# Optimization experiments

Measured on AMD Instinct MI355X. Metric: run time of the kernel, lower is better.

## Reference

```python
import jax, jax.numpy as jnp
import numpy as np

K = 3
UP_H, UP_W = 120, 160  # up_size
RES_H, RES_W = UP_H + K - 1, UP_W + K - 1  # bilinear target before valid depthwise conv


def _bilinear_align_corners(x, out_h, out_w):
    """PyTorch UpsamplingBilinear2d (align_corners=True). x: [B,C,H,W]."""
    B, C, H, W = x.shape
    # row interpolation
    hy = jnp.arange(out_h, dtype=x.dtype) * ((H - 1) / (out_h - 1))
    y0 = jnp.floor(hy).astype(jnp.int32)
    y1 = jnp.minimum(y0 + 1, H - 1)
    fy = (hy - y0.astype(x.dtype))[None, None, :, None]
    x = x[:, :, y0, :] * (1 - fy) + x[:, :, y1, :] * fy  # [B,C,out_h,W]
    # col interpolation
    wx = jnp.arange(out_w, dtype=x.dtype) * ((W - 1) / (out_w - 1))
    x0i = jnp.floor(wx).astype(jnp.int32)
    x1i = jnp.minimum(x0i + 1, W - 1)
    fx = (wx - x0i.astype(x.dtype))[None, None, None, :]
    return x[:, :, :, x0i] * (1 - fx) + x[:, :, :, x1i] * fx  # [B,C,out_h,out_w]


def setup_inputs() -> dict:
    key = jax.random.key(0)
    k1, k2, k3 = jax.random.split(key, 3)
    C_in, C_out = 256, 128
    x = jax.random.normal(k1, (8, C_in, 60, 80), dtype=jnp.float32)
    # depthwise kernel [C_in, 1, K, K], pointwise [C_out, C_in]; fan-in-ish scale
    w_dw = jax.random.normal(k2, (C_in, 1, K, K), dtype=jnp.float32) * (1.0 / K)
    w_pw = jax.random.normal(k3, (C_out, C_in), dtype=jnp.float32) * (1.0 / np.sqrt(C_in))
    return {"x": x, "w_dw": w_dw, "w_pw": w_pw}


def reference(x, w_dw, w_pw):
    C_in = x.shape[1]
    # 1) bilinear upsample (align_corners=True) to (UP_H+K-1, UP_W+K-1)
    up = _bilinear_align_corners(x, RES_H, RES_W)
    # 2) depthwise KxK conv, stride 1, VALID padding -> [B,C_in,UP_H,UP_W]
    dw = jax.lax.conv_general_dilated(
        up, w_dw, window_strides=(1, 1), padding="VALID",
        dimension_numbers=("NCHW", "OIHW", "NCHW"),
        feature_group_count=C_in)
    # 3) pointwise 1x1 conv -> [B,C_out,UP_H,UP_W]
    return jnp.einsum("bchw,oc->bohw", dw, w_pw)
```

## Files before the change

kernel.cpp:

```cpp
#include <hip/hip_runtime.h>

#define CIN  256
#define HIN  60
#define WIN  80
#define UPH  120
#define UPW  160
#define COUT 128
#define NPIX (UPH*UPW)

typedef __bf16 bf16x2 __attribute__((ext_vector_type(2)));
typedef __bf16 bf16x8 __attribute__((ext_vector_type(8)));
typedef float  floatx4 __attribute__((ext_vector_type(4)));

#define A_NT 320
#define A_XR 5
#define A_CP 17
#define A_AS 49

__global__ __launch_bounds__(A_NT, 5) void dw_kernel(
    const float* __restrict__ x,
    const float* __restrict__ wdw,
    __bf16* __restrict__ dwb,
    int b0)
{
    __shared__ bf16x2 s_px[A_XR * 84 * A_CP];
    __shared__ float  s_A[16 * A_AS];

    const int tid = threadIdx.x;
    const int h0  = blockIdx.x * 4;
    const int cb  = blockIdx.y * 16;
    const int bl  = blockIdx.z;
    const int b   = b0 + bl;

    const float HS = 59.0f / 121.0f;
    const float WS = 79.0f / 161.0f;
    const int rbase = (int)(h0 * HS);

    const float* xb = x + ((size_t)b * CIN + cb) * (HIN * WIN);
    #pragma unroll
    for (int k = 0; k < 6; k++) {
        int i = tid + k * A_NT;
        if (i < 1680) {
            int ch  = i / 105;
            int rem = i - ch * 105;
            int r   = rem / 21;
            int c4  = rem - r * 21;
            int gy  = min(rbase + r, HIN - 1);
            const float* xrow = xb + (size_t)ch * (HIN * WIN) + gy * WIN;
            int base = (r * 84 + c4 * 4) * A_CP + ch;
            if (c4 < 20) {
                float4 v = *(const float4*)(xrow + c4 * 4);
                float x5 = xrow[min(c4 * 4 + 4, WIN - 1)];
                s_px[base]          = (bf16x2){(__bf16)v.x, (__bf16)v.y};
                s_px[base + A_CP]   = (bf16x2){(__bf16)v.y, (__bf16)v.z};
                s_px[base + 2*A_CP] = (bf16x2){(__bf16)v.z, (__bf16)v.w};
                s_px[base + 3*A_CP] = (bf16x2){(__bf16)v.w, (__bf16)x5};
            } else {
                float v = xrow[WIN - 1];
                bf16x2 p = {(__bf16)v, (__bf16)v};
                s_px[base]          = p;
                s_px[base + A_CP]   = p;
                s_px[base + 2*A_CP] = p;
                s_px[base + 3*A_CP] = p;
            }
        }
    }
    for (int i = tid; i < 16 * 4 * 9; i += A_NT) {
        int ch  = i / 36;
        int rem = i - ch * 36;
        int h   = rem / 9;
        int dyj = rem - h * 9;
        int dy  = dyj / 3;
        int j   = dyj - dy * 3;
        int ybh = (int)((h0 + h) * HS);
        float acc = 0.f;
        #pragma unroll
        for (int i3 = 0; i3 < 3; i3++) {
            float hy = (h0 + h + i3) * HS;
            int y0 = (int)hy;
            float fy = hy - (float)y0;
            int y1 = min(y0 + 1, HIN - 1);
            float wgt = ((y0 - ybh) == dy ? (1.f - fy) : 0.f)
                      + ((y1 - ybh) == dy ? fy : 0.f);
            acc = fmaf(wgt, wdw[(cb + ch) * 9 + i3 * 3 + j], acc);
        }
        s_A[ch * A_AS + h * 12 + dy * 4 + j] = acc;
    }
    __syncthreads();

    const int ch  = tid & 15;
    const int rid = tid >> 4;
    const int wq  = rid * 8;
    int rbh[4];
    #pragma unroll
    for (int hh = 0; hh < 4; hh++)
        rbh[hh] = (int)((h0 + hh) * HS) - rbase;

    float fx[10]; int wi[10];
    #pragma unroll
    for (int j = 0; j < 10; j++) {
        float wx = (float)(wq + j) * WS;
        int x0 = (int)wx;
        fx[j] = wx - (float)x0;
        wi[j] = x0 * A_CP + ch;
    }

    float d[4][8];
    #pragma unroll
    for (int hh = 0; hh < 4; hh++)
        #pragma unroll
        for (int i = 0; i < 8; i++) d[hh][i] = 0.f;

    #pragma unroll
    for (int r = 0; r < A_XR; r++) {
        float cx[10];
        #pragma unroll
        for (int j = 0; j < 10; j++) {
            bf16x2 p = s_px[r * 84 * A_CP + wi[j]];
            float lo = (float)p[0], hi = (float)p[1];
            cx[j] = fmaf(fx[j], hi - lo, lo);
        }
        #pragma unroll
        for (int hh = 0; hh < 4; hh++) {
            int dyL = r - rbh[hh];
            if ((unsigned)dyL <= 2u) {
                const float* Ab = &s_A[ch * A_AS + hh * 12 + dyL * 4];
                float A0 = Ab[0], A1 = Ab[1], A2 = Ab[2];
                #pragma unroll
                for (int i = 0; i < 8; i++)
                    d[hh][i] = fmaf(A0, cx[i],
                               fmaf(A1, cx[i+1],
                               fmaf(A2, cx[i+2], d[hh][i])));
            }
        }
    }
    #pragma unroll
    for (int hh = 0; hh < 4; hh++) {
        bf16x8 o;
        #pragma unroll
        for (int i = 0; i < 8; i++) o[i] = (__bf16)d[hh][i];
        size_t off = ((size_t)bl * CIN + cb + ch) * NPIX
                   + (size_t)(h0 + hh) * UPW + wq;
        *(bf16x8*)(dwb + off) = o;
    }
}

#define B_NT 512
#define B_WS 264
#define B_DS 40

__global__ __launch_bounds__(B_NT, 4) void pw_kernel(
    const __bf16* __restrict__ dwb,
    const float* __restrict__ wpw,
    float* __restrict__ out,
    int b0)
{
    __shared__ __align__(16) __bf16 s_wpw[COUT * B_WS];
    __shared__ __align__(16) __bf16 s_dw[128 * B_DS];

    const int tid  = threadIdx.x;
    const int tile = blockIdx.x;
    const int bl   = blockIdx.y;
    const int b    = b0 + bl;

    {
        const int o = tid >> 2, seg = tid & 3;
        #pragma unroll
        for (int q = 0; q < 8; q++) {
            int c0 = seg * 64 + q * 8;
            float4 v0 = *(const float4*)(wpw + (size_t)o * CIN + c0);
            float4 v1 = *(const float4*)(wpw + (size_t)o * CIN + c0 + 4);
            bf16x8 f = {(__bf16)v0.x, (__bf16)v0.y, (__bf16)v0.z, (__bf16)v0.w,
                        (__bf16)v1.x, (__bf16)v1.y, (__bf16)v1.z, (__bf16)v1.w};
            *(bf16x8*)&s_wpw[o * B_WS + c0] = f;
        }
    }

    const int wave = tid >> 6, lane = tid & 63;
    const int quad = lane >> 4, l16 = lane & 15;
    const int o32  = (wave & 3) * 32;
    const int pg   = wave >> 2;

    floatx4 acc[2][4];
    #pragma unroll
    for (int a = 0; a < 2; a++)
        #pragma unroll
        for (int p = 0; p < 4; p++) acc[a][p] = (floatx4){0.f,0.f,0.f,0.f};

    const __bf16* dwbase = dwb + (size_t)bl * CIN * NPIX + tile * 128;
    const int cS = tid & 31, p8 = tid >> 5;

    bf16x8 v = *(const bf16x8*)(dwbase + (size_t)cS * NPIX + p8 * 8);

    for (int ck = 0; ck < 8; ck++) {
        __syncthreads();
        #pragma unroll
        for (int i = 0; i < 8; i++)
            s_dw[(p8 * 8 + i) * B_DS + cS] = v[i];
        __syncthreads();

        if (ck < 7)
            v = *(const bf16x8*)(dwbase + (size_t)((ck+1) * 32 + cS) * NPIX + p8 * 8);

        bf16x8 af0 = *(const bf16x8*)&s_wpw[(o32 + l16) * B_WS + ck * 32 + quad * 8];
        bf16x8 af1 = *(const bf16x8*)&s_wpw[(o32 + 16 + l16) * B_WS + ck * 32 + quad * 8];
        #pragma unroll
        for (int pt = 0; pt < 4; pt++) {
            bf16x8 bf = *(const bf16x8*)&s_dw[(pg * 64 + pt * 16 + l16) * B_DS + quad * 8];
            acc[0][pt] = __builtin_amdgcn_mfma_f32_16x16x32_bf16(af0, bf, acc[0][pt], 0, 0, 0);
            acc[1][pt] = __builtin_amdgcn_mfma_f32_16x16x32_bf16(af1, bf, acc[1][pt], 0, 0, 0);
        }
    }

    float* ob = out + (size_t)b * COUT * NPIX + tile * 128;
    #pragma unroll
    for (int ot = 0; ot < 2; ot++)
        #pragma unroll
        for (int pt = 0; pt < 4; pt++)
            #pragma unroll
            for (int r = 0; r < 4; r++)
                ob[(size_t)(o32 + ot * 16 + quad * 4 + r) * NPIX
                   + pg * 64 + pt * 16 + l16] = acc[ot][pt][r];
}

extern "C" void kernel_launch(void* const* d_in, const int* in_sizes, int n_in,
                              void* d_out, int out_size, void* d_ws, size_t ws_size,
                              hipStream_t stream) {
    const float* x   = (const float*)d_in[0];
    const float* wdw = (const float*)d_in[1];
    const float* wpw = (const float*)d_in[2];
    float* out = (float*)d_out;
    __bf16* dwb = (__bf16*)d_ws;

    int bs = 8;
    while (bs > 1 && (size_t)bs * CIN * NPIX * 2 > ws_size) bs >>= 1;

    for (int b0 = 0; b0 < 8; b0 += bs) {
        dim3 gA(30, CIN / 16, bs);
        dw_kernel<<<gA, A_NT, 0, stream>>>(x, wdw, dwb, b0);
        dim3 gB(NPIX / 128, bs);
        pw_kernel<<<gB, B_NT, 0, stream>>>(dwb, wpw, out, b0);
    }
}
```

Before: 203.0 us.

## Fuse depthwise upsample-conv and pointwise MFMA GEMM into one kernel

Replaces the two-kernel pipeline, which wrote the bf16 depthwise intermediate to global workspace and read it back, with a single fused kernel. Each block computes a 4x32 pixel tile's depthwise output for 64 channels at a time into double-buffered shared memory and immediately feeds it to MFMA for the pointwise conv. A small pre-kernel converts the pointwise weights to bf16 once. This removes the global round-trip of the intermediate but recomputes the per-channel weight table per tile and loads the weight fragments from global inside the loop.

```diff
diff --git a/kernel.cpp b/kernel.cpp
--- a/kernel.cpp
+++ b/kernel.cpp
@@ -12,233 +12,228 @@
 typedef __bf16 bf16x8 __attribute__((ext_vector_type(8)));
 typedef float  floatx4 __attribute__((ext_vector_type(4)));
 
-#define A_NT 320
-#define A_XR 5
-#define A_CP 17
-#define A_AS 49
-
-__global__ __launch_bounds__(A_NT, 5) void dw_kernel(
+__global__ void wpw_cvt(const float* __restrict__ wpw, __bf16* __restrict__ wpwb)
+{
+    int i = (blockIdx.x * blockDim.x + threadIdx.x) * 8;
+    float4 a = *(const float4*)(wpw + i);
+    float4 b = *(const float4*)(wpw + i + 4);
+    bf16x8 o = {(__bf16)a.x,(__bf16)a.y,(__bf16)a.z,(__bf16)a.w,
+                (__bf16)b.x,(__bf16)b.y,(__bf16)b.z,(__bf16)b.w};
+    *(bf16x8*)(wpwb + i) = o;
+}
+
+#define F_NT 512
+#define KC   64
+#define NCK  (CIN/KC)
+#define PXR  5
+#define PXW  20
+#define DWS  72
+#define AST  37
+
+__global__ __launch_bounds__(F_NT, 4) void fused_kernel(
     const float* __restrict__ x,
     const float* __restrict__ wdw,
-    __bf16* __restrict__ dwb,
-    int b0)
+    const __bf16* __restrict__ wpwb,
+    float* __restrict__ out)
 {
-    __shared__ bf16x2 s_px[A_XR * 84 * A_CP];
-    __shared__ float  s_A[16 * A_AS];
+    __shared__ bf16x2 s_px[PXR*PXW*64];
+    __shared__ __bf16 s_dw[2][128*DWS];
+    __shared__ float  s_A[64*AST];
+    __shared__ float  s_rw[36];
 
     const int tid = threadIdx.x;
-    const int h0  = blockIdx.x * 4;
-    const int cb  = blockIdx.y * 16;
-    const int bl  = blockIdx.z;
-    const int b   = b0 + bl;
-
-    const float HS = 59.0f / 121.0f;
-    const float WS = 79.0f / 161.0f;
-    const int rbase = (int)(h0 * HS);
-
-    const float* xb = x + ((size_t)b * CIN + cb) * (HIN * WIN);
-    #pragma unroll
-    for (int k = 0; k < 6; k++) {
-        int i = tid + k * A_NT;
-        if (i < 1680) {
-            int ch  = i / 105;
-            int rem = i - ch * 105;
-            int r   = rem / 21;
-            int c4  = rem - r * 21;
-            int gy  = min(rbase + r, HIN - 1);
-            const float* xrow = xb + (size_t)ch * (HIN * WIN) + gy * WIN;
-            int base = (r * 84 + c4 * 4) * A_CP + ch;
-            if (c4 < 20) {
-                float4 v = *(const float4*)(xrow + c4 * 4);
-                float x5 = xrow[min(c4 * 4 + 4, WIN - 1)];
-                s_px[base]          = (bf16x2){(__bf16)v.x, (__bf16)v.y};
-                s_px[base + A_CP]   = (bf16x2){(__bf16)v.y, (__bf16)v.z};
-                s_px[base + 2*A_CP] = (bf16x2){(__bf16)v.z, (__bf16)v.w};
-                s_px[base + 3*A_CP] = (bf16x2){(__bf16)v.w, (__bf16)x5};
-            } else {
-                float v = xrow[WIN - 1];
-                bf16x2 p = {(__bf16)v, (__bf16)v};
-                s_px[base]          = p;
-                s_px[base + A_CP]   = p;
-                s_px[base + 2*A_CP] = p;
-                s_px[base + 3*A_CP] = p;
-            }
-        }
+    const int wt = blockIdx.x, ht = blockIdx.y, b = blockIdx.z;
+    const int h0 = ht*4, w0 = wt*32;
+
+    const float HS = 59.0f/121.0f, WS = 79.0f/161.0f;
+    const int rbase = (int)((float)h0*HS);
+    const int c0 = (int)((float)w0*WS);
+
+    if (tid < 36) {
+        int hh = tid/9, t = tid - hh*9;
+        int i3 = t/3, dy = t - i3*3;
+        int ybh = (int)((float)(h0+hh)*HS);
+        float hy = (float)(h0+hh+i3)*HS;
+        int y0 = (int)hy; float fy = hy - (float)y0;
+        int y1 = min(y0+1, HIN-1);
+        s_rw[tid] = ((y0-ybh)==dy ? 1.f-fy : 0.f) + ((y1-ybh)==dy ? fy : 0.f);
     }
-    for (int i = tid; i < 16 * 4 * 9; i += A_NT) {
-        int ch  = i / 36;
-        int rem = i - ch * 36;
-        int h   = rem / 9;
-        int dyj = rem - h * 9;
-        int dy  = dyj / 3;
-        int j   = dyj - dy * 3;
-        int ybh = (int)((h0 + h) * HS);
-        float acc = 0.f;
-        #pragma unroll
-        for (int i3 = 0; i3 < 3; i3++) {
-            float hy = (h0 + h + i3) * HS;
-            int y0 = (int)hy;
-            float fy = hy - (float)y0;
-            int y1 = min(y0 + 1, HIN - 1);
-            float wgt = ((y0 - ybh) == dy ? (1.f - fy) : 0.f)
-                      + ((y1 - ybh) == dy ? fy : 0.f);
-            acc = fmaf(wgt, wdw[(cb + ch) * 9 + i3 * 3 + j], acc);
-        }
-        s_A[ch * A_AS + h * 12 + dy * 4 + j] = acc;
-    }
-    __syncthreads();
-
-    const int ch  = tid & 15;
-    const int rid = tid >> 4;
-    const int wq  = rid * 8;
-    int rbh[4];
-    #pragma unroll
-    for (int hh = 0; hh < 4; hh++)
-        rbh[hh] = (int)((h0 + hh) * HS) - rbase;
+
+    const int cl = tid & 63;
+    const int wseg = (tid>>6)&3;
+    const int hp = tid>>8;
+    const int hh0 = hp*2;
+    const int rl0 = (int)((float)(h0+hh0)*HS) - rbase;
+    const int dd  = ((int)((float)(h0+hh0+1)*HS) - rbase) - rl0;
 
     float fx[10]; int wi[10];
     #pragma unroll
     for (int j = 0; j < 10; j++) {
-        float wx = (float)(wq + j) * WS;
+        float wx = (float)(w0 + wseg*8 + j) * WS;
         int x0 = (int)wx;
         fx[j] = wx - (float)x0;
-        wi[j] = x0 * A_CP + ch;
+        wi[j] = (x0 - c0)*64 + cl;
     }
 
-    float d[4][8];
+    const int lane = tid & 63, wave = tid >> 6;
+    const int quad = lane >> 4, l16 = lane & 15;
+    const int co = (wave & 3)*32, phx = (wave >> 2)*64;
+
+    floatx4 acc[2][4];
     #pragma unroll
-    for (int hh = 0; hh < 4; hh++)
-        #pragma unroll
-        for (int i = 0; i < 8; i++) d[hh][i] = 0.f;
-
-    #pragma unroll
-    for (int r = 0; r < A_XR; r++) {
-        float cx[10];
-        #pragma unroll
-        for (int j = 0; j < 10; j++) {
-            bf16x2 p = s_px[r * 84 * A_CP + wi[j]];
-            float lo = (float)p[0], hi = (float)p[1];
-            cx[j] = fmaf(fx[j], hi - lo, lo);
-        }
-        #pragma unroll
-        for (int hh = 0; hh < 4; hh++) {
-            int dyL = r - rbh[hh];
-            if ((unsigned)dyL <= 2u) {
-                const float* Ab = &s_A[ch * A_AS + hh * 12 + dyL * 4];
+    for (int a = 0; a < 2; a++)
+        #pragma unroll
+        for (int p = 0; p < 4; p++) acc[a][p] = (floatx4){0.f,0.f,0.f,0.f};
+
+    const float* xb = x + (size_t)b * CIN * (HIN*WIN);
+
+    __syncthreads();
+
+    for (int ck = 0; ck < NCK; ck++) {
+        const int cb = ck * KC;
+
+        #pragma unroll
+        for (int k = 0; k < 4; k++) {
+            int i = tid + k*F_NT;
+            if (i < 1600) {
+                int ch = i & 63, rq = i >> 6;
+                int r = rq/5, q = rq - r*5;
+                int gy = min(rbase + r, HIN-1);
+                const float* xrow = xb + (size_t)(cb+ch)*(HIN*WIN) + gy*WIN;
+                int cq = c0 + q*4;
+                int base = (r*PXW + q*4)*64 + ch;
+                if (cq + 4 <= WIN-1) {
+                    float4 v = *(const float4*)(xrow + cq);
+                    float x5 = xrow[cq+4];
+                    s_px[base       ] = (bf16x2){(__bf16)v.x,(__bf16)v.y};
+                    s_px[base +   64] = (bf16x2){(__bf16)v.y,(__bf16)v.z};
+                    s_px[base + 2*64] = (bf16x2){(__bf16)v.z,(__bf16)v.w};
+                    s_px[base + 3*64] = (bf16x2){(__bf16)v.w,(__bf16)x5};
+                } else {
+                    float f[5];
+                    #pragma unroll
+                    for (int kk = 0; kk < 5; kk++) f[kk] = xrow[min(cq+kk, WIN-1)];
+                    #pragma unroll
+                    for (int kk = 0; kk < 4; kk++)
+                        s_px[base + kk*64] = (bf16x2){(__bf16)f[kk],(__bf16)f[kk+1]};
+                }
+            }
+        }
+
+        #pragma unroll
+        for (int k = 0; k < 5; k++) {
+            int i = tid + k*F_NT;
+            if (i < 2304) {
+                int ci = i & 63, t = i >> 6;
+                int hh = t/9, dyj = t - hh*9, dy = dyj/3, j = dyj - dy*3;
+                const float* wp = wdw + (size_t)(cb+ci)*9 + j;
+                float a = s_rw[hh*9 + dy]     * wp[0]
+                        + s_rw[hh*9 + 3 + dy] * wp[3]
+                        + s_rw[hh*9 + 6 + dy] * wp[6];
+                s_A[ci*AST + t] = a;
+            }
+        }
+
+        __syncthreads();
+
+        __bf16* dwp = s_dw[ck & 1];
+        float d0[8], d1[8];
+        #pragma unroll
+        for (int i = 0; i < 8; i++) { d0[i] = 0.f; d1[i] = 0.f; }
+
+        #pragma unroll
+        for (int rr = 0; rr < 3; rr++) {
+            int r = rl0 + rr;
+            float cx[10];
+            #pragma unroll
+            for (int j = 0; j < 10; j++) {
+                bf16x2 p = s_px[r*(PXW*64) + wi[j]];
+                float lo = (float)p[0], hi = (float)p[1];
+                cx[j] = fmaf(fx[j], hi - lo, lo);
+            }
+            {
+                const float* Ab = &s_A[cl*AST + hh0*9 + rr*3];
                 float A0 = Ab[0], A1 = Ab[1], A2 = Ab[2];
                 #pragma unroll
                 for (int i = 0; i < 8; i++)
-                    d[hh][i] = fmaf(A0, cx[i],
-                               fmaf(A1, cx[i+1],
-                               fmaf(A2, cx[i+2], d[hh][i])));
-            }
+                    d0[i] = fmaf(A0, cx[i], fmaf(A1, cx[i+1], fmaf(A2, cx[i+2], d0[i])));
+            }
+            int dyL = rr - dd;
+            if ((unsigned)dyL <= 2u) {
+                const float* Ab = &s_A[cl*AST + (hh0+1)*9 + dyL*3];
+                float A0 = Ab[0], A1 = Ab[1], A2 = Ab[2];
+                #pragma unroll
+                for (int i = 0; i < 8; i++)
+                    d1[i] = fmaf(A0, cx[i], fmaf(A1, cx[i+1], fmaf(A2, cx[i+2], d1[i])));
+            }
+        }
+        if (dd) {
+            int r = rl0 + 3;
+            float cx[10];
+            #pragma unroll
+            for (int j = 0; j < 10; j++) {
+                bf16x2 p = s_px[r*(PXW*64) + wi[j]];
+                float lo = (float)p[0], hi = (float)p[1];
+                cx[j] = fmaf(fx[j], hi - lo, lo);
+            }
+            const float* Ab = &s_A[cl*AST + (hh0+1)*9 + 2*3];
+            float A0 = Ab[0], A1 = Ab[1], A2 = Ab[2];
+            #pragma unroll
+            for (int i = 0; i < 8; i++)
+                d1[i] = fmaf(A0, cx[i], fmaf(A1, cx[i+1], fmaf(A2, cx[i+2], d1[i])));
+        }
+
+        {
+            int pxb0 = (hh0*32 + wseg*8)*DWS + cl;
+            int pxb1 = pxb0 + 32*DWS;
+            #pragma unroll
+            for (int i = 0; i < 8; i++) {
+                dwp[pxb0 + i*DWS] = (__bf16)d0[i];
+                dwp[pxb1 + i*DWS] = (__bf16)d1[i];
+            }
+        }
+
+        const __bf16* wrow = wpwb + (size_t)(co + l16)*CIN + cb + quad*8;
+        bf16x8 af00 = *(const bf16x8*)(wrow);
+        bf16x8 af01 = *(const bf16x8*)(wrow + 32);
+        bf16x8 af10 = *(const bf16x8*)(wrow + 16*CIN);
+        bf16x8 af11 = *(const bf16x8*)(wrow + 16*CIN + 32);
+
+        __syncthreads();
+
+        #pragma unroll
+        for (int pt = 0; pt < 4; pt++) {
+            const __bf16* bp = &dwp[(phx + pt*16 + l16)*DWS + quad*8];
+            bf16x8 bf0 = *(const bf16x8*)(bp);
+            bf16x8 bf1 = *(const bf16x8*)(bp + 32);
+            acc[0][pt] = __builtin_amdgcn_mfma_f32_16x16x32_bf16(af00, bf0, acc[0][pt], 0,0,0);
+            acc[0][pt] = __builtin_amdgcn_mfma_f32_16x16x32_bf16(af01, bf1, acc[0][pt], 0,0,0);
+            acc[1][pt] = __builtin_amdgcn_mfma_f32_16x16x32_bf16(af10, bf0, acc[1][pt], 0,0,0);
+            acc[1][pt] = __builtin_amdgcn_mfma_f32_16x16x32_bf16(af11, bf1, acc[1][pt], 0,0,0);
         }
     }
-    #pragma unroll
-    for (int hh = 0; hh < 4; hh++) {
-        bf16x8 o;
-        #pragma unroll
-        for (int i = 0; i < 8; i++) o[i] = (__bf16)d[hh][i];
-        size_t off = ((size_t)bl * CIN + cb + ch) * NPIX
-                   + (size_t)(h0 + hh) * UPW + wq;
-        *(bf16x8*)(dwb + off) = o;
-    }
-}
-
-#define B_NT 512
-#define B_WS 264
-#define B_DS 40
-
-__global__ __launch_bounds__(B_NT, 4) void pw_kernel(
-    const __bf16* __restrict__ dwb,
-    const float* __restrict__ wpw,
-    float* __restrict__ out,
-    int b0)
-{
-    __shared__ __align__(16) __bf16 s_wpw[COUT * B_WS];
-    __shared__ __align__(16) __bf16 s_dw[128 * B_DS];
-
-    const int tid  = threadIdx.x;
-    const int tile = blockIdx.x;
-    const int bl   = blockIdx.y;
-    const int b    = b0 + bl;
-
-    {
-        const int o = tid >> 2, seg = tid & 3;
-        #pragma unroll
-        for (int q = 0; q < 8; q++) {
-            int c0 = seg * 64 + q * 8;
-            float4 v0 = *(const float4*)(wpw + (size_t)o * CIN + c0);
-            float4 v1 = *(const float4*)(wpw + (size_t)o * CIN + c0 + 4);
-            bf16x8 f = {(__bf16)v0.x, (__bf16)v0.y, (__bf16)v0.z, (__bf16)v0.w,
-                        (__bf16)v1.x, (__bf16)v1.y, (__bf16)v1.z, (__bf16)v1.w};
-            *(bf16x8*)&s_wpw[o * B_WS + c0] = f;
-        }
-    }
-
-    const int wave = tid >> 6, lane = tid & 63;
-    const int quad = lane >> 4, l16 = lane & 15;
-    const int o32  = (wave & 3) * 32;
-    const int pg   = wave >> 2;
-
-    floatx4 acc[2][4];
-    #pragma unroll
-    for (int a = 0; a < 2; a++)
-        #pragma unroll
-        for (int p = 0; p < 4; p++) acc[a][p] = (floatx4){0.f,0.f,0.f,0.f};
-
-    const __bf16* dwbase = dwb + (size_t)bl * CIN * NPIX + tile * 128;
-    const int cS = tid & 31, p8 = tid >> 5;
-
-    bf16x8 v = *(const bf16x8*)(dwbase + (size_t)cS * NPIX + p8 * 8);
-
-    for (int ck = 0; ck < 8; ck++) {
-        __syncthreads();
-        #pragma unroll
-        for (int i = 0; i < 8; i++)
-            s_dw[(p8 * 8 + i) * B_DS + cS] = v[i];
-        __syncthreads();
-
-        if (ck < 7)
-            v = *(const bf16x8*)(dwbase + (size_t)((ck+1) * 32 + cS) * NPIX + p8 * 8);
-
-        bf16x8 af0 = *(const bf16x8*)&s_wpw[(o32 + l16) * B_WS + ck * 32 + quad * 8];
-        bf16x8 af1 = *(const bf16x8*)&s_wpw[(o32 + 16 + l16) * B_WS + ck * 32 + quad * 8];
-        #pragma unroll
-        for (int pt = 0; pt < 4; pt++) {
-            bf16x8 bf = *(const bf16x8*)&s_dw[(pg * 64 + pt * 16 + l16) * B_DS + quad * 8];
-            acc[0][pt] = __builtin_amdgcn_mfma_f32_16x16x32_bf16(af0, bf, acc[0][pt], 0, 0, 0);
-            acc[1][pt] = __builtin_amdgcn_mfma_f32_16x16x32_bf16(af1, bf, acc[1][pt], 0, 0, 0);
-        }
-    }
-
-    float* ob = out + (size_t)b * COUT * NPIX + tile * 128;
+
+    float* ob = out + ((size_t)b*COUT + co)*NPIX + (size_t)h0*UPW + w0;
     #pragma unroll
     for (int ot = 0; ot < 2; ot++)
         #pragma unroll
-        for (int pt = 0; pt < 4; pt++)
-            #pragma unroll
-            for (int r = 0; r < 4; r++)
-                ob[(size_t)(o32 + ot * 16 + quad * 4 + r) * NPIX
-                   + pg * 64 + pt * 16 + l16] = acc[ot][pt][r];
+        for (int pt = 0; pt < 4; pt++) {
+            int px = phx + pt*16 + l16;
+            float* p = ob + (size_t)(ot*16 + quad*4)*NPIX + (px>>5)*UPW + (px&31);
+            #pragma unroll
+            for (int e = 0; e < 4; e++) p[(size_t)e*NPIX] = acc[ot][pt][e];
+        }
 }
 
 extern "C" void kernel_launch(void* const* d_in, const int* in_sizes, int n_in,
                               void* d_out, int out_size, void* d_ws, size_t ws_size,
-                              hipStream_t stream) {
+                              hipStream_t stream)
+{
     const float* x   = (const float*)d_in[0];
     const float* wdw = (const float*)d_in[1];
     const float* wpw = (const float*)d_in[2];
-    float* out = (float*)d_out;
-    __bf16* dwb = (__bf16*)d_ws;
-
-    int bs = 8;
-    while (bs > 1 && (size_t)bs * CIN * NPIX * 2 > ws_size) bs >>= 1;
-
-    for (int b0 = 0; b0 < 8; b0 += bs) {
-        dim3 gA(30, CIN / 16, bs);
-        dw_kernel<<<gA, A_NT, 0, stream>>>(x, wdw, dwb, b0);
-        dim3 gB(NPIX / 128, bs);
-        pw_kernel<<<gB, B_NT, 0, stream>>>(dwb, wpw, out, b0);
-    }
+
+    wpw_cvt<<<dim3((COUT*CIN)/(256*8)), 256, 0, stream>>>(wpw, (__bf16*)d_ws);
+    fused_kernel<<<dim3(UPW/32, UPH/4, 8), F_NT, 0, stream>>>(
+        x, wdw, (const __bf16*)d_ws, (float*)d_out);
 }
```

Measured after the change: 323.6 us. +59.5%, slower.
